# Performance work log

Hardware: AMD Instinct MI355X
Metric: run time of the kernel (lower is better)

## Reference

```python
import jax, jax.numpy as jnp
import numpy as np

B, BOUNDS, NRIM, K, UNITS = 4096, 512, 6, 4, 600
H_IN, DK_IN, DV_IN = 4, 64, 400
H_C, DK_C, DV_C = 4, 32, 100


def setup_inputs() -> dict:
    key = jax.random.key(0)
    ks = jax.random.split(key, 16)
    s = 0.02
    return {
        'inputs': jax.random.normal(ks[0], (B, BOUNDS + NRIM), jnp.float32),
        'hs': jax.random.normal(ks[1], (B, NRIM, UNITS), jnp.float32) * s,
        'cs': jax.random.normal(ks[2], (B, NRIM, UNITS), jnp.float32) * s,
        'Wk': jax.random.normal(ks[3], (BOUNDS, H_IN * DK_IN), jnp.float32) * s,
        'bk': jnp.zeros((H_IN * DK_IN,), jnp.float32),
        'Wv': jax.random.normal(ks[4], (BOUNDS, H_IN * DV_IN), jnp.float32) * s,
        'bv': jnp.zeros((H_IN * DV_IN,), jnp.float32),
        'Wq': jax.random.normal(ks[5], (NRIM, UNITS, H_IN * DK_IN), jnp.float32) * s,
        'lstm_k': jax.random.normal(ks[6], (NRIM, DV_IN, 4 * UNITS), jnp.float32) * s,
        'lstm_r': jax.random.normal(ks[7], (NRIM, UNITS, 4 * UNITS), jnp.float32) * s,
        'lstm_b': jnp.zeros((NRIM, 4 * UNITS), jnp.float32),
        'Wkc': jax.random.normal(ks[8], (NRIM, UNITS, H_C * DK_C), jnp.float32) * s,
        'Wvc': jax.random.normal(ks[9], (NRIM, UNITS, H_C * DV_C), jnp.float32) * s,
        'Wqc': jax.random.normal(ks[10], (NRIM, UNITS, H_C * DK_C), jnp.float32) * s,
        'Wout': jax.random.normal(ks[11], (NRIM, H_C * DV_C, UNITS), jnp.float32) * s,
    }


def _split_heads(t, n_heads, d_head):
    # [B, T, n_heads*d_head] -> [B, n_heads, T, d_head] (matches tf.split+stack)
    b, t_len = t.shape[0], t.shape[1]
    return t.reshape(b, t_len, n_heads, d_head).transpose(0, 2, 1, 3)


def reference(inputs, hs, cs, Wk, bk, Wv, bv, Wq, lstm_k, lstm_r, lstm_b, Wkc, Wvc, Wqc, Wout):
    x = inputs[:, :BOUNDS]                                   # [B, bounds]
    rim_dist = inputs[:, BOUNDS:BOUNDS + NRIM]               # [B, nRIM]

    # ---- input attention ----
    xx = jnp.stack([x, jnp.zeros_like(x)], axis=1)           # [B, 2, bounds]
    k_lay = xx @ Wk + bk                                     # [B, 2, H*dk]
    v_lay = xx @ Wv + bv                                     # [B, 2, H*dv]
    q_lay = jnp.einsum('bnu,nuo->bno', hs, Wq)               # grouped linear [B, nRIM, H*dq]
    kh = _split_heads(k_lay, H_IN, DK_IN)                    # [B, H, 2, dk]
    vh = _split_heads(v_lay, H_IN, DV_IN)                    # [B, H, 2, dv]
    qh = _split_heads(q_lay, H_IN, DK_IN)                    # [B, H, nRIM, dk]
    v2 = vh.mean(axis=1)                                     # [B, 2, dv]
    scores = jnp.einsum('bhnd,bhtd->bhnt', qh, kh) / np.sqrt(DK_IN).astype(np.float32)
    scores2 = scores.mean(axis=1)                            # [B, nRIM, 2]

    # top-k RIM selection mask from RIM_dist (use_attn=False path)
    _, idx = jax.lax.top_k(rim_dist, K)                      # [B, K]
    mask = jnp.zeros((inputs.shape[0], NRIM), inputs.dtype)
    mask = mask.at[jnp.arange(inputs.shape[0])[:, None], idx].set(1.0)[..., None]  # [B, nRIM, 1]

    probs = jax.nn.softmax(scores2, axis=-1)                 # dropout inactive (training=False)
    rnn_in = jnp.einsum('bnt,btv->bnv', probs, v2) * mask    # [B, nRIM, dv]

    # ---- grouped LSTM (keras gate order i,f,c,o) ----
    gates = (jnp.einsum('bnv,nvo->bno', rnn_in, lstm_k)
             + jnp.einsum('bnu,nuo->bno', hs, lstm_r) + lstm_b)  # [B, nRIM, 4*units]
    i, f, g, o = jnp.split(gates, 4, axis=-1)
    c_rnn = jax.nn.sigmoid(f) * cs + jax.nn.sigmoid(i) * jnp.tanh(g)
    h_rnn = jax.nn.sigmoid(o) * jnp.tanh(c_rnn)
    h_new = jax.lax.stop_gradient(h_rnn * (1.0 - mask)) + h_rnn * mask

    # ---- communication attention among RIMs ----
    kc = _split_heads(jnp.einsum('bnu,nuo->bno', h_new, Wkc), H_C, DK_C)  # [B, Hc, nRIM, dkc]
    vc = _split_heads(jnp.einsum('bnu,nuo->bno', h_new, Wvc), H_C, DV_C)
    qc = _split_heads(jnp.einsum('bnu,nuo->bno', h_new, Wqc), H_C, DK_C)
    sc = jnp.einsum('bhnd,bhmd->bhnm', qc, kc) / np.sqrt(DK_C).astype(np.float32)
    pc = jax.nn.softmax(sc, axis=-1) * mask[:, None, :, :]   # zero rows of inactive query RIMs
    ctx = jnp.einsum('bhnm,bhmv->bhnv', pc, vc)              # [B, Hc, nRIM, dvc]
    ctx = ctx.transpose(0, 2, 1, 3).reshape(inputs.shape[0], NRIM, H_C * DV_C)
    h_comm = jnp.einsum('bno,nou->bnu', ctx, Wout) + h_new   # grouped output proj + residual

    # ---- masked state update ----
    h_upd = h_comm * mask + hs * (1.0 - mask)
    c_upd = c_rnn * mask + cs * (1.0 - mask)
    out_state = h_upd.reshape(inputs.shape[0], UNITS * NRIM)
    return out_state, h_upd, c_upd
```

## Files before the change

### kernel.cpp

```cpp
#include <hip/hip_runtime.h>

namespace {
typedef unsigned short u16;
typedef __attribute__((ext_vector_type(8))) __bf16 bf16x8;
typedef __attribute__((ext_vector_type(4))) float f32x4;

constexpr long long kB  = 4096;
constexpr long long kOS = kB * 3600;
constexpr size_t kGAs = 4096ull * 1088;
constexpr int kHnS = 3648;

constexpr size_t oWkvT  = 0;
constexpr size_t oWqT   = oWkvT  + 768ull*512*2;
constexpr size_t oWcomT = oWqT   + 6ull*256*640*2;
constexpr size_t oWoutT = oWcomT + 6ull*768*640*2;
constexpr size_t oLstmT = oWoutT + 6ull*640*448*2;
constexpr size_t oBp    = oLstmT + 6ull*2560*1024*2;
constexpr size_t oBkv   = oBp    + 6ull*2560*4;
constexpr size_t oMask  = oBkv   + 768*4;
constexpr size_t oArena = oMask  + 4096ull*6*4;
constexpr size_t oGA    = oArena;
constexpr size_t oKV    = oGA   + 6ull*kGAs*2;
constexpr size_t oXbf   = oKV   + 4096ull*768*2;
constexpr size_t oQlay  = oXbf;
constexpr size_t oCqv   = oArena;
constexpr size_t oCtx   = oCqv  + 4096ull*4608*2;
}

__device__ __forceinline__ u16 f2b(float f) {
  union { float f; unsigned u; } x; x.f = f;
  unsigned r = (x.u + 0x7fffu + ((x.u >> 16) & 1u)) >> 16;
  return (u16)r;
}
__device__ __forceinline__ float b2f(u16 u) {
  union { unsigned u; float f; } x; x.u = ((unsigned)u) << 16;
  return x.f;
}
__device__ __forceinline__ float sigmoidf_(float x) { return 1.f / (1.f + __expf(-x)); }
__device__ __forceinline__ float tanhf_(float x) {
  const float e = __expf(2.f * x);
  return 1.f - 2.f / (e + 1.f);
}

__device__ __forceinline__ void gload16(const void* g, void* l) {
  __builtin_amdgcn_global_load_lds((const __attribute__((address_space(1))) void*)g,
                                   (__attribute__((address_space(3))) void*)l, 16, 0, 0);
}

union FragU4 { uint4 u4; bf16x8 v; };

template<int MODE>
__global__ __launch_bounds__(256, 2) void gemm64(
    const u16* __restrict__ A, int lda, long strideA,
    const u16* __restrict__ Bt, long strideB, int Kpad,
    void* __restrict__ C, int ldc, int strideC,
    const float* __restrict__ bias, int strideBias,
    int N, int nks, int storeBf16, int nx,
    const float* __restrict__ mask, float* __restrict__ h_upd,
    const float* __restrict__ hs_in, float* __restrict__ out_state)
{
  __shared__ __align__(16) u16 lds[2 * 16384];

  const int nwg = gridDim.x;
  const int orig = blockIdx.x;
  int wgid;
  {
    const int q = nwg >> 3, r = nwg & 7;
    const int xcd = orig & 7, bidx = orig >> 3;
    wgid = (xcd < r ? xcd * (q + 1) : r * (q + 1) + (xcd - r) * q) + bidx;
  }
  const int xt = wgid % nx;
  const int t2 = wgid / nx;
  const int mt = t2 & 31;
  const int rim = t2 >> 5;
  const int m0 = mt * 128, n0 = xt * 128;

  A += (size_t)rim * strideA;
  Bt += (size_t)rim * strideB;
  if (bias) bias += (size_t)rim * strideBias;

  const int t = threadIdx.x;
  const int w = t >> 6, lane = t & 63;
  const int lrow = lane & 15, lk = lane >> 4;
  const int wr = w >> 1, wc = w & 1;

  f32x4 acc[4][4] = {};

  const u16* aS[4]; const u16* bS[4]; int cC[4];
#pragma unroll
  for (int i = 0; i < 4; ++i) {
    const int c = t + i * 256;
    const int row = c >> 3, slot = c & 7;
    cC[i] = c;
    aS[i] = A  + (size_t)(m0 + row) * lda  + ((slot ^ (row & 7)) << 3);
    bS[i] = Bt + (size_t)(n0 + row) * Kpad + ((slot ^ (row & 7)) << 3);
  }
  auto stage = [&](u16* dst) {
#pragma unroll
    for (int i = 0; i < 4; ++i) gload16(aS[i], dst + (size_t)cC[i] * 8);
#pragma unroll
    for (int i = 0; i < 4; ++i) gload16(bS[i], dst + 8192 + (size_t)cC[i] * 8);
#pragma unroll
    for (int i = 0; i < 4; ++i) { aS[i] += 64; bS[i] += 64; }
  };

  stage(lds);
  asm volatile("s_waitcnt vmcnt(0)" ::: "memory");
  __builtin_amdgcn_s_barrier();

  for (int s = 0; s < nks; ++s) {
    const bool more = (s + 1 < nks);
    if (more) stage(lds + ((s + 1) & 1) * 16384);
    __builtin_amdgcn_sched_barrier(0);
    const char* Ab = (const char*)(lds + (s & 1) * 16384);
    const char* Bb = Ab + 16384;
#pragma unroll
    for (int ks = 0; ks < 2; ++ks) {
      FragU4 af[4], bf4[4];
#pragma unroll
      for (int mf = 0; mf < 4; ++mf) {
        const int rr = wr * 64 + mf * 16 + lrow;
        af[mf].u4 = *(const uint4*)(Ab + rr * 128 + ((((ks << 2) | lk) ^ (rr & 7)) << 4));
      }
#pragma unroll
      for (int nf = 0; nf < 4; ++nf) {
        const int rr = wc * 64 + nf * 16 + lrow;
        bf4[nf].u4 = *(const uint4*)(Bb + rr * 128 + ((((ks << 2) | lk) ^ (rr & 7)) << 4));
      }
#pragma unroll
      for (int mf = 0; mf < 4; ++mf)
#pragma unroll
        for (int nf = 0; nf < 4; ++nf)
          acc[mf][nf] = __builtin_amdgcn_mfma_f32_16x16x32_bf16(af[mf].v, bf4[nf].v, acc[mf][nf], 0, 0, 0);
    }
    if (more) {
      asm volatile("s_waitcnt vmcnt(0)" ::: "memory");
      __builtin_amdgcn_s_barrier();
    }
  }

  if (MODE == 0) {
    float* Cf = (float*)C + (size_t)rim * strideC;
    u16*   Cu = (u16*)C + (size_t)rim * strideC;
#pragma unroll
    for (int mf = 0; mf < 4; ++mf)
#pragma unroll
      for (int r2 = 0; r2 < 4; ++r2) {
        const int m = m0 + wr * 64 + mf * 16 + 4 * lk + r2;
#pragma unroll
        for (int nf = 0; nf < 4; ++nf) {
          const int col = n0 + wc * 64 + nf * 16 + lrow;
          if (col < N) {
            float v = acc[mf][nf][r2];
            if (bias) v += bias[col];
            const size_t off = (size_t)m * ldc + col;
            if (storeBf16) Cu[off] = f2b(v); else Cf[off] = v;
          }
        }
      }
  } else {
#pragma unroll
    for (int mf = 0; mf < 4; ++mf)
#pragma unroll
      for (int r2 = 0; r2 < 4; ++r2) {
        const int m = m0 + wr * 64 + mf * 16 + 4 * lk + r2;
        const float mk = mask[(size_t)m * 6 + rim];
#pragma unroll
        for (int nf = 0; nf < 4; ++nf) {
          const int col = n0 + wc * 64 + nf * 16 + lrow;
          if (col < 600) {
            const size_t off = (size_t)m * 3600 + rim * 600 + col;
            const float v = (mk != 0.f) ? (acc[mf][nf][r2] + h_upd[off]) : hs_in[off];
            h_upd[off] = v;
            out_state[off] = v;
          }
        }
      }
  }
}

__global__ __launch_bounds__(512, 2) void gates256(
    const u16* __restrict__ A, const u16* __restrict__ Bt,
    const float* __restrict__ bp, const float* __restrict__ cs,
    const float* __restrict__ mask,
    float* __restrict__ c_upd, float* __restrict__ h_upd, u16* __restrict__ hnbf)
{
  __shared__ __align__(16) u16 lds[2 * 32768];

  const int orig = blockIdx.x;
  const int wgid = (orig & 7) * 120 + (orig >> 3);
  const int rim = wgid / 160;
  const int rem = wgid % 160;
  const int half = rem / 80;
  const int r2d = rem % 80;
  const int mt = r2d / 5;
  const int xt = half * 5 + r2d % 5;
  const int m0 = mt * 256, n0 = xt * 256;

  const u16* Ar = A + (size_t)rim * kGAs;
  const u16* Br = Bt + (size_t)rim * (2560ull * 1024);
  const float* bip = bp + (size_t)rim * 2560;

  const int t = threadIdx.x;
  const int w = t >> 6, lane = t & 63;
  const int lrow = lane & 15, lk = lane >> 4;
  const int wr = w >> 2, wc = w & 3;

  f32x4 acc[8][4] = {};

  const u16* aP[2]; const u16* bP[2]; int dC[2];
#pragma unroll
  for (int i = 0; i < 2; ++i) {
    const int c = t + i * 512;
    const int grow = 2 * (c >> 3) + ((c >> 2) & 1);
    const int su2 = (c & 3) ^ ((c >> 3) & 3);
    dC[i] = c * 8;
    aP[i] = Ar + (size_t)(m0 + grow) * 1088 + su2 * 8;
    bP[i] = Br + (size_t)(n0 + grow) * 1024 + su2 * 8;
  }
  auto stageU = [&](int isB, int kh, int ktile, u16* buf) {
    u16* dst = buf + (isB ? 16384 : 0) + kh * 8192;
    const int go = ktile * 64 + kh * 32;
#pragma unroll
    for (int i = 0; i < 2; ++i)
      gload16((isB ? bP[i] : aP[i]) + go, dst + dC[i]);
  };

  constexpr int nks = 16;
  stageU(0, 0, 0, lds); stageU(1, 0, 0, lds); stageU(0, 1, 0, lds); stageU(1, 1, 0, lds);

  for (int T = 0; T < nks; ++T) {
    const char* tb = (const char*)(lds + (T & 1) * 32768);
    const char* Ah[2] = { tb, tb + 16384 };
    const char* Bh[2] = { tb + 32768, tb + 49152 };
    u16* nxt = lds + ((T + 1) & 1) * 32768;
    const bool st = (T + 1 < nks);

    FragU4 af[4], bfr[4];

    asm volatile("s_waitcnt vmcnt(4)\ns_barrier" ::: "memory");
    __builtin_amdgcn_sched_barrier(0);
#pragma unroll
    for (int nf = 0; nf < 4; ++nf) {
      const int rr = wc * 64 + nf * 16 + lrow;
      bfr[nf].u4 = *(const uint4*)(Bh[0] + (rr >> 1) * 128 +
                   ((((rr & 1) << 2) | (lk ^ ((rr >> 1) & 3))) << 4));
    }
#pragma unroll
    for (int mf = 0; mf < 4; ++mf) {
      const int rr = wr * 128 + mf * 16 + lrow;
      af[mf].u4 = *(const uint4*)(Ah[0] + (rr >> 1) * 128 +
                  ((((rr & 1) << 2) | (lk ^ ((rr >> 1) & 3))) << 4));
    }
    if (st) stageU(0, 0, T + 1, nxt);
    __builtin_amdgcn_s_setprio(1);
#pragma unroll
    for (int mf = 0; mf < 4; ++mf)
#pragma unroll
      for (int nf = 0; nf < 4; ++nf)
        acc[mf][nf] = __builtin_amdgcn_mfma_f32_16x16x32_bf16(af[mf].v, bfr[nf].v, acc[mf][nf], 0, 0, 0);
    __builtin_amdgcn_s_setprio(0);

#pragma unroll
    for (int mf = 0; mf < 4; ++mf) {
      const int rr = wr * 128 + 64 + mf * 16 + lrow;
      af[mf].u4 = *(const uint4*)(Ah[0] + (rr >> 1) * 128 +
                  ((((rr & 1) << 2) | (lk ^ ((rr >> 1) & 3))) << 4));
    }
    if (st) stageU(1, 0, T + 1, nxt);
    __builtin_amdgcn_s_setprio(1);
#pragma unroll
    for (int mf = 0; mf < 4; ++mf)
#pragma unroll
      for (int nf = 0; nf < 4; ++nf)
        acc[4 + mf][nf] = __builtin_amdgcn_mfma_f32_16x16x32_bf16(af[mf].v, bfr[nf].v, acc[4 + mf][nf], 0, 0, 0);
    __builtin_amdgcn_s_setprio(0);

    if (st) asm volatile("s_waitcnt vmcnt(4)\ns_barrier" ::: "memory");
    else    asm volatile("s_waitcnt vmcnt(0)\ns_barrier" ::: "memory");
    __builtin_amdgcn_sched_barrier(0);
#pragma unroll
    for (int nf = 0; nf < 4; ++nf) {
      const int rr = wc * 64 + nf * 16 + lrow;
      bfr[nf].u4 = *(const uint4*)(Bh[1] + (rr >> 1) * 128 +
                   ((((rr & 1) << 2) | (lk ^ ((rr >> 1) & 3))) << 4));
    }
#pragma unroll
    for (int mf = 0; mf < 4; ++mf) {
      const int rr = wr * 128 + mf * 16 + lrow;
      af[mf].u4 = *(const uint4*)(Ah[1] + (rr >> 1) * 128 +
                  ((((rr & 1) << 2) | (lk ^ ((rr >> 1) & 3))) << 4));
    }
    if (st) stageU(0, 1, T + 1, nxt);
    __builtin_amdgcn_s_setprio(1);
#pragma unroll
    for (int mf = 0; mf < 4; ++mf)
#pragma unroll
      for (int nf = 0; nf < 4; ++nf)
        acc[mf][nf] = __builtin_amdgcn_mfma_f32_16x16x32_bf16(af[mf].v, bfr[nf].v, acc[mf][nf], 0, 0, 0);
    __builtin_amdgcn_s_setprio(0);

#pragma unroll
    for (int mf = 0; mf < 4; ++mf) {
      const int rr = wr * 128 + 64 + mf * 16 + lrow;
      af[mf].u4 = *(const uint4*)(Ah[1] + (rr >> 1) * 128 +
                  ((((rr & 1) << 2) | (lk ^ ((rr >> 1) & 3))) << 4));
    }
    if (st) stageU(1, 1, T + 1, nxt);
    __builtin_amdgcn_s_setprio(1);
#pragma unroll
    for (int mf = 0; mf < 4; ++mf)
#pragma unroll
      for (int nf = 0; nf < 4; ++nf)
        acc[4 + mf][nf] = __builtin_amdgcn_mfma_f32_16x16x32_bf16(af[mf].v, bfr[nf].v, acc[4 + mf][nf], 0, 0, 0);
    __builtin_amdgcn_s_setprio(0);
  }

  const int nb = n0 + wc * 64;
  const int u = ((nb >> 6) << 4) + lrow;
  if (u < 600) {
    const float b_i = bip[nb + lrow];
    const float b_f = bip[nb + 16 + lrow];
    const float b_g = bip[nb + 32 + lrow];
    const float b_o = bip[nb + 48 + lrow];
#pragma unroll
    for (int mf = 0; mf < 8; ++mf)
#pragma unroll
      for (int r2 = 0; r2 < 4; ++r2) {
        const int m = m0 + wr * 128 + mf * 16 + 4 * lk + r2;
        const float iv = acc[mf][0][r2] + b_i;
        const float fv = acc[mf][1][r2] + b_f;
        const float gv = acc[mf][2][r2] + b_g;
        const float ov = acc[mf][3][r2] + b_o;
        const size_t off = (size_t)m * 3600 + rim * 600 + u;
        const float cprev = cs[off];
        const float cv = sigmoidf_(fv) * cprev + sigmoidf_(iv) * tanhf_(gv);
        const float hv = sigmoidf_(ov) * tanhf_(cv);
        const float mk = mask[(size_t)m * 6 + rim];
        c_upd[off] = (mk != 0.f) ? cv : cprev;
        h_upd[off] = hv;
        hnbf[(size_t)m * kHnS + rim * 600 + u] = f2b(hv);
      }
  }
}

__device__ void pack_wt_body(float (*tile)[65], int bx, int by, int rim,
    const float* __restrict__ i1, long s1, const float* __restrict__ i2, long s2,
    int K1, int Ktot, int ldin, int Nreal,
    u16* __restrict__ out, long so, int Kpad, int gateperm, int tid)
{
  i1 += (size_t)rim * s1;
  if (i2) i2 += (size_t)rim * s2;
  u16* o = out + (size_t)rim * so;
  const int n0 = bx * 64, k0 = by * 64;
  const int lane = tid & 63, qq = tid >> 6;
  const int n = n0 + lane;
  int col;
  if (gateperm) {
    const int g = (n >> 4) & 3, u = ((n >> 6) << 4) + (n & 15);
    col = (u < 600) ? g * 600 + u : -1;
  } else {
    col = (n < Nreal) ? n : -1;
  }
#pragma unroll
  for (int i = 0; i < 16; ++i) {
    const int kk = qq + 4 * i;
    const int k = k0 + kk;
    float v = 0.f;
    if (col >= 0) {
      if (k < K1) v = i1[(size_t)k * ldin + col];
      else if (k < Ktot) v = i2[(size_t)(k - K1) * ldin + col];
    }
    tile[kk][lane] = v;
  }
  __syncthreads();
#pragma unroll
  for (int i = 0; i < 16; ++i) {
    const int nn = qq + 4 * i;
    const int k = k0 + lane;
    if (k < Kpad) o[(size_t)(n0 + nn) * Kpad + k] = f2b(tile[lane][nn]);
  }
}

__global__ __launch_bounds__(256) void megapack_w(
    const float* __restrict__ Wk, const float* __restrict__ Wv,
    const float* __restrict__ Wkc, const float* __restrict__ Wqc, const float* __restrict__ Wvc,
    const float* __restrict__ Wq, const float* __restrict__ Wout,
    const float* __restrict__ lstm_k, const float* __restrict__ lstm_r,
    u16* __restrict__ WkvT, u16* __restrict__ WcomT, u16* __restrict__ WqT,
    u16* __restrict__ WoutT, u16* __restrict__ LstmT)
{
  __shared__ float tile[64][65];
  const int id = blockIdx.x, t = threadIdx.x;
  if (id < 3840) {
    const int bx = id % 40, by = (id / 40) % 16, bz = id / 640;
    pack_wt_body(tile, bx, by, bz, lstm_k, 400l*2400, lstm_r, 600l*2400,
                 400, 1000, 2400, 2400, LstmT, 2560l*1024, 1024, 1, t);
  } else if (id < 4260) {
    const int i2 = id - 3840;
    const int bx = i2 % 10, by = (i2 / 10) % 7, bz = i2 / 70;
    pack_wt_body(tile, bx, by, bz, Wout, 400l*600, nullptr, 0,
                 400, 400, 600, 600, WoutT, 640l*448, 448, 0, t);
  } else if (id < 4500) {
    const int i3 = id - 4260;
    const int bx = i3 % 4, by = (i3 / 4) % 10, bz = i3 / 40;
    pack_wt_body(tile, bx, by, bz, Wq, 600l*256, nullptr, 0,
                 600, 600, 256, 256, WqT, 256l*640, 640, 0, t);
  } else if (id < 4692) {
    const int e8 = ((id - 4500) * 256 + t) * 8;
    const int n = e8 >> 9, k0 = e8 & 511;
    u16 st[8];
#pragma unroll
    for (int j = 0; j < 8; ++j) {
      const int k = k0 + j;
      float v = 0.f;
      if (n < 256) v = Wk[(size_t)k * 256 + n];
      else if (n < 656) {
        const float* p = Wv + (size_t)k * 1600 + (n - 256);
        v = 0.25f * (p[0] + p[400] + p[800] + p[1200]);
      }
      st[j] = f2b(v);
    }
    *(uint4*)(WkvT + e8) = *(const uint4*)st;
  } else {
    const long long e8 = ((long long)(id - 4692) * 256 + t) * 8;
    const int rim = (int)(e8 / 491520);
    const int rem = (int)(e8 % 491520);
    const int n = rem / 640, k0 = rem % 640;
    u16 st[8];
#pragma unroll
    for (int j = 0; j < 8; ++j) {
      const int k = k0 + j;
      float v = 0.f;
      if (k < 600) {
        if (n < 128)      v = Wkc[(size_t)rim * 76800 + (size_t)k * 128 + n];
        else if (n < 256) v = Wqc[(size_t)rim * 76800 + (size_t)k * 128 + (n - 128)];
        else if (n < 656) v = Wvc[(size_t)rim * 240000 + (size_t)k * 400 + (n - 256)];
      }
      st[j] = f2b(v);
    }
    *(uint4*)(WcomT + e8) = *(const uint4*)st;
  }
}

__global__ __launch_bounds__(256) void megapack_act(
    const float* __restrict__ inputs, const float* __restrict__ hs,
    const float* __restrict__ lstm_b, const float* __restrict__ bk, const float* __restrict__ bv,
    u16* __restrict__ xbf, u16* __restrict__ gA, float* __restrict__ bp, float* __restrict__ bkv,
    u16* __restrict__ hnbf)
{
  __shared__ float row[3600];
  const int id = blockIdx.x, t = threadIdx.x;
  if (id < 4096) {
    const int b = id;
    for (int i = t; i < 3600; i += 256) row[i] = hs[(size_t)b * 3600 + i];
    __syncthreads();
    for (int c = t; c < 516; c += 256) {
      const int rim = c / 86;
      const int j = (c % 86) * 8;
      u16 v[8];
#pragma unroll
      for (int k = 0; k < 8; ++k) {
        const int col = j + k;
        v[k] = (col < 600) ? f2b(row[rim * 600 + col]) : (u16)0;
      }
      *(uint4*)(gA + (size_t)rim * kGAs + (size_t)b * 1088 + 400 + j) = *(const uint4*)v;
    }
    if (t < 6) {
      u16 z[8] = {0,0,0,0,0,0,0,0};
      *(uint4*)(hnbf + (size_t)b * kHnS + 3600 + t * 8) = *(const uint4*)z;
    }
  } else if (id < 5120) {
    const int e8 = ((id - 4096) * 256 + t) * 8;
    const int b = e8 >> 9, c0 = e8 & 511;
    const float* src = inputs + (size_t)b * 518 + c0;
    u16 st[8];
#pragma unroll
    for (int j = 0; j < 8; ++j) st[j] = f2b(src[j]);
    *(uint4*)(xbf + e8) = *(const uint4*)st;
  } else {
    const int tt = (id - 5120) * 256 + t;
    if (tt < 6 * 2560) {
      const int rim = tt / 2560, p = tt % 2560;
      const int g = (p >> 4) & 3, u = ((p >> 6) << 4) + (p & 15);
      bp[tt] = (u < 600) ? lstm_b[(size_t)rim * 2400 + g * 600 + u] : 0.f;
    }
    if (tt < 768) {
      float v = 0.f;
      if (tt < 256) v = bk[tt];
      else if (tt < 656) { const int j2 = tt - 256; v = 0.25f * (bv[j2] + bv[j2+400] + bv[j2+800] + bv[j2+1200]); }
      bkv[tt] = v;
    }
  }
}

__global__ __launch_bounds__(256) void score_kernel(
    const float* __restrict__ inputs, const u16* __restrict__ qlayb,
    const u16* __restrict__ kvb, const float* __restrict__ bk,
    const float* __restrict__ bkv,
    float* __restrict__ maskout, u16* __restrict__ gA)
{
  const int b = blockIdx.x;
  const int t = threadIdx.x;
  __shared__ float red[4][12];
  __shared__ float sprob[12];
  __shared__ float smask[6];

  const float k0v = b2f(kvb[(size_t)b * 768 + t]);
  const float bkv_ = bk[t];
  float part[12];
#pragma unroll
  for (int n = 0; n < 6; ++n) {
    const float q = b2f(qlayb[(size_t)b * 1536 + n * 256 + t]);
    part[2 * n]     = q * k0v;
    part[2 * n + 1] = q * bkv_;
  }
#pragma unroll
  for (int off = 32; off > 0; off >>= 1)
#pragma unroll
    for (int i = 0; i < 12; ++i)
      part[i] += __shfl_down(part[i], off);
  const int wave = t >> 6, lane = t & 63;
  if (lane == 0)
#pragma unroll
    for (int i = 0; i < 12; ++i) red[wave][i] = part[i];
  __syncthreads();
  if (t < 12) red[0][t] = (red[0][t] + red[1][t] + red[2][t] + red[3][t]) * (1.0f / 32.0f);
  __syncthreads();
  if (t < 6) {
    const float s0 = red[0][2 * t], s1 = red[0][2 * t + 1];
    const float mx = fmaxf(s0, s1);
    const float e0 = __expf(s0 - mx), e1 = __expf(s1 - mx);
    const float inv = 1.f / (e0 + e1);
    sprob[2 * t] = e0 * inv;
    sprob[2 * t + 1] = e1 * inv;
    const float* rd = inputs + (size_t)b * 518 + 512;
    const float mine = rd[t];
    int rank = 0;
#pragma unroll
    for (int j = 0; j < 6; ++j) {
      const float o = rd[j];
      rank += (o > mine) || (o == mine && j < t);
    }
    const float mk = (rank < 4) ? 1.f : 0.f;
    smask[t] = mk;
    maskout[(size_t)b * 6 + t] = mk;
  }
  __syncthreads();
  for (int c = t; c < 300; c += 256) {
    const int n = c / 50;
    const int v = (c % 50) * 8;
    const float p0 = sprob[2 * n], p1 = sprob[2 * n + 1], mk = smask[n];
    u16 st[8];
#pragma unroll
    for (int k = 0; k < 8; ++k)
      st[k] = f2b((p0 * b2f(kvb[(size_t)b * 768 + 256 + v + k]) + p1 * bkv[256 + v + k]) * mk);
    *reinterpret_cast<uint4*>(gA + (size_t)n * kGAs + (size_t)b * 1088 + v) =
        *reinterpret_cast<const uint4*>(st);
  }
}

__global__ __launch_bounds__(256) void comm_kernel(
    const u16* __restrict__ cqv, u16* __restrict__ ctx)
{
  const int b = blockIdx.x, t = threadIdx.x;
  __shared__ float skc[768], sqc[768], svc[2400];
  __shared__ float spc[4][6][6];
  for (int i = t * 4; i < 4608; i += 1024) {
    const ushort4 u4 = *reinterpret_cast<const ushort4*>(cqv + (size_t)b * 4608 + i);
    const u16 uu[4] = {u4.x, u4.y, u4.z, u4.w};
#pragma unroll
    for (int j = 0; j < 4; ++j) {
      const int ii = i + j;
      const int m = ii / 768, c = ii % 768;
      const float v = b2f(uu[j]);
      if (c < 128) skc[m * 128 + c] = v;
      else if (c < 256) sqc[m * 128 + (c - 128)] = v;
      else if (c < 656) svc[m * 400 + (c - 256)] = v;
    }
  }
  __syncthreads();
  if (t < 144) {
    const int h = t / 36, n = (t % 36) / 6, m = t % 6;
    float s = 0.f;
#pragma unroll
    for (int d = 0; d < 32; ++d) s += sqc[n * 128 + h * 32 + d] * skc[m * 128 + h * 32 + d];
    spc[h][n][m] = s * 0.17677669529663687f;
  }
  __syncthreads();
  if (t < 24) {
    const int h = t / 6, n = t % 6;
    float mx = -3.0e38f;
#pragma unroll
    for (int m = 0; m < 6; ++m) mx = fmaxf(mx, spc[h][n][m]);
    float e[6], sum = 0.f;
#pragma unroll
    for (int m = 0; m < 6; ++m) { e[m] = __expf(spc[h][n][m] - mx); sum += e[m]; }
    const float inv = 1.f / sum;
#pragma unroll
    for (int m = 0; m < 6; ++m) spc[h][n][m] = e[m] * inv;
  }
  __syncthreads();
  for (int base = t * 4; base < 2400; base += 1024) {
    const int n = base / 400, rr = base % 400, h = rr / 100, v = rr % 100;
    ushort4 st;
    float s0 = 0.f, s1 = 0.f, s2 = 0.f, s3 = 0.f;
#pragma unroll
    for (int m = 0; m < 6; ++m) {
      const float p = spc[h][n][m];
      const float* vm = &svc[m * 400 + h * 100 + v];
      s0 += p * vm[0]; s1 += p * vm[1]; s2 += p * vm[2]; s3 += p * vm[3];
    }
    st.x = f2b(s0); st.y = f2b(s1); st.z = f2b(s2); st.w = f2b(s3);
    *reinterpret_cast<ushort4*>(ctx + (size_t)b * 2400 + base) = st;
  }
}

extern "C" void kernel_launch(void* const* d_in, const int* in_sizes, int n_in,
                              void* d_out, int out_size, void* d_ws, size_t ws_size,
                              hipStream_t stream) {
  const float* inputs = (const float*)d_in[0];
  const float* hs     = (const float*)d_in[1];
  const float* cs     = (const float*)d_in[2];
  const float* Wk     = (const float*)d_in[3];
  const float* bk     = (const float*)d_in[4];
  const float* Wv     = (const float*)d_in[5];
  const float* bv     = (const float*)d_in[6];
  const float* Wq     = (const float*)d_in[7];
  const float* lstm_k = (const float*)d_in[8];
  const float* lstm_r = (const float*)d_in[9];
  const float* lstm_b = (const float*)d_in[10];
  const float* Wkc    = (const float*)d_in[11];
  const float* Wvc    = (const float*)d_in[12];
  const float* Wqc    = (const float*)d_in[13];
  const float* Wout   = (const float*)d_in[14];

  float* out = (float*)d_out;
  float* out_state = out;
  float* h_upd = out + kOS;
  float* c_upd = out + 2 * kOS;
  u16*   hnbf  = (u16*)d_out;

  char* wsb = (char*)d_ws;
  u16* WkvT  = (u16*)(wsb + oWkvT);
  u16* WqT   = (u16*)(wsb + oWqT);
  u16* WcomT = (u16*)(wsb + oWcomT);
  u16* WoutT = (u16*)(wsb + oWoutT);
  u16* LstmT = (u16*)(wsb + oLstmT);
  float* bp    = (float*)(wsb + oBp);
  float* bkv   = (float*)(wsb + oBkv);
  float* maskf = (float*)(wsb + oMask);
  u16* gA    = (u16*)(wsb + oGA);
  u16* kvb   = (u16*)(wsb + oKV);
  u16* xbf   = (u16*)(wsb + oXbf);
  u16* qlayb = (u16*)(wsb + oQlay);
  u16* cqvb  = (u16*)(wsb + oCqv);
  u16* ctxb  = (u16*)(wsb + oCtx);

  dim3 B256(256);

  megapack_w<<<6132, B256, 0, stream>>>(Wk, Wv, Wkc, Wqc, Wvc, Wq, Wout, lstm_k, lstm_r,
                                        WkvT, WcomT, WqT, WoutT, LstmT);
  megapack_act<<<5180, B256, 0, stream>>>(inputs, hs, lstm_b, bk, bv, xbf, gA, bp, bkv, hnbf);

  gemm64<0><<<dim3(192), B256, 0, stream>>>(xbf, 512, 0, WkvT, 0, 512,
      kvb, 768, 0, bkv, 0, 656, 8, 1, 6,
      nullptr, nullptr, nullptr, nullptr);
  gemm64<0><<<dim3(384), B256, 0, stream>>>(gA + 400, 1088, (long)kGAs, WqT, 256l*640, 640,
      qlayb, 1536, 256, nullptr, 0, 256, 10, 1, 2,
      nullptr, nullptr, nullptr, nullptr);

  score_kernel<<<4096, B256, 0, stream>>>(inputs, qlayb, kvb, bk, bkv, maskf, gA);

  gates256<<<dim3(960), dim3(512), 0, stream>>>(gA, LstmT, bp, cs, maskf, c_upd, h_upd, hnbf);

  gemm64<0><<<dim3(1152), B256, 0, stream>>>(hnbf, kHnS, 600, WcomT, 768l*640, 640,
      cqvb, 4608, 768, nullptr, 0, 656, 10, 1, 6,
      nullptr, nullptr, nullptr, nullptr);

  comm_kernel<<<4096, B256, 0, stream>>>(cqvb, ctxb);

  gemm64<1><<<dim3(960), B256, 0, stream>>>(ctxb, 2400, 400, WoutT, 640l*448, 448,
      nullptr, 0, 0, nullptr, 0, 600, 7, 0, 5,
      maskf, h_upd, hs, out_state);
}
```

Baseline: 563.0 us.

## Split A-tile staging per half and add finer-grained waits in LSTM GEMM

Reorganizes the LSTM gate GEMM's LDS staging so each A half-tile (64 rows) is loaded separately with a simpler row-linear swizzled layout, and B is staged alongside the first A half. Extra s_waitcnt/barrier points are inserted before each half's fragment reads, so the kernel waits only for the data it needs next instead of a whole k-slice. This aims to overlap global loads with MFMA work more tightly and simplify LDS address math. The cost is additional barriers per iteration and vmcnt bookkeeping that must exactly match the issue order, which is easy to get wrong.

```diff
diff --git a/kernel.cpp b/kernel.cpp
--- a/kernel.cpp
+++ b/kernel.cpp
@@ -208,51 +208,52 @@
 
   f32x4 acc[8][4] = {};
 
-  const u16* aP[2]; const u16* bP[2]; int dC[2];
+  const int aR = ((t >> 2) & 63) + (((t >> 2) >> 6) << 7);
+  const int aSu = (t & 3) ^ ((t >> 3) & 3);
+  const u16* aBase = Ar + (size_t)(m0 + aR) * 1088 + aSu * 8;
+  const u16* bBase[2];
 #pragma unroll
   for (int i = 0; i < 2; ++i) {
     const int c = t + i * 512;
-    const int grow = 2 * (c >> 3) + ((c >> 2) & 1);
-    const int su2 = (c & 3) ^ ((c >> 3) & 3);
-    dC[i] = c * 8;
-    aP[i] = Ar + (size_t)(m0 + grow) * 1088 + su2 * 8;
-    bP[i] = Br + (size_t)(n0 + grow) * 1024 + su2 * 8;
-  }
-  auto stageU = [&](int isB, int kh, int ktile, u16* buf) {
-    u16* dst = buf + (isB ? 16384 : 0) + kh * 8192;
-    const int go = ktile * 64 + kh * 32;
-#pragma unroll
-    for (int i = 0; i < 2; ++i)
-      gload16((isB ? bP[i] : aP[i]) + go, dst + dC[i]);
+    const int row = c >> 2;
+    const int su = (c & 3) ^ ((c >> 3) & 3);
+    bBase[i] = Br + (size_t)(n0 + row) * 1024 + su * 8;
+  }
+  auto stageA = [&](int h, int ks, int Tt, u16* buf) {
+    gload16(aBase + (size_t)h * 64 * 1088 + Tt * 64 + ks * 32,
+            buf + (ks * 2 + h) * 4096 + t * 8);
   };
+  auto stageB = [&](int ks, int Tt, u16* buf) {
+    gload16(bBase[0] + Tt * 64 + ks * 32, buf + 16384 + ks * 8192 + t * 8);
+    gload16(bBase[1] + Tt * 64 + ks * 32, buf + 16384 + ks * 8192 + (t + 512) * 8);
+  };
 
   constexpr int nks = 16;
-  stageU(0, 0, 0, lds); stageU(1, 0, 0, lds); stageU(0, 1, 0, lds); stageU(1, 1, 0, lds);
+  stageA(0, 0, 0, lds); stageB(0, 0, lds);
+  stageA(1, 0, 0, lds);
+  stageA(0, 1, 0, lds); stageB(1, 0, lds);
+  stageA(1, 1, 0, lds);
 
   for (int T = 0; T < nks; ++T) {
     const char* tb = (const char*)(lds + (T & 1) * 32768);
-    const char* Ah[2] = { tb, tb + 16384 };
-    const char* Bh[2] = { tb + 32768, tb + 49152 };
     u16* nxt = lds + ((T + 1) & 1) * 32768;
     const bool st = (T + 1 < nks);
 
     FragU4 af[4], bfr[4];
 
-    asm volatile("s_waitcnt vmcnt(4)\ns_barrier" ::: "memory");
+    asm volatile("s_waitcnt vmcnt(5)\ns_barrier" ::: "memory");
     __builtin_amdgcn_sched_barrier(0);
 #pragma unroll
     for (int nf = 0; nf < 4; ++nf) {
       const int rr = wc * 64 + nf * 16 + lrow;
-      bfr[nf].u4 = *(const uint4*)(Bh[0] + (rr >> 1) * 128 +
-                   ((((rr & 1) << 2) | (lk ^ ((rr >> 1) & 3))) << 4));
+      bfr[nf].u4 = *(const uint4*)(tb + 32768 + rr * 64 + ((lk ^ ((rr >> 1) & 3)) << 4));
     }
 #pragma unroll
     for (int mf = 0; mf < 4; ++mf) {
-      const int rr = wr * 128 + mf * 16 + lrow;
-      af[mf].u4 = *(const uint4*)(Ah[0] + (rr >> 1) * 128 +
-                  ((((rr & 1) << 2) | (lk ^ ((rr >> 1) & 3))) << 4));
-    }
-    if (st) stageU(0, 0, T + 1, nxt);
+      const int rp = wr * 64 + mf * 16 + lrow;
+      af[mf].u4 = *(const uint4*)(tb + rp * 64 + ((lk ^ ((rp >> 1) & 3)) << 4));
+    }
+    if (st) { stageA(0, 0, T + 1, nxt); stageB(0, T + 1, nxt); }
     __builtin_amdgcn_s_setprio(1);
 #pragma unroll
     for (int mf = 0; mf < 4; ++mf)
@@ -261,13 +262,15 @@
         acc[mf][nf] = __builtin_amdgcn_mfma_f32_16x16x32_bf16(af[mf].v, bfr[nf].v, acc[mf][nf], 0, 0, 0);
     __builtin_amdgcn_s_setprio(0);
 
+    if (st) asm volatile("s_waitcnt vmcnt(7)\ns_barrier" ::: "memory");
+    else    asm volatile("s_waitcnt vmcnt(4)\ns_barrier" ::: "memory");
+    __builtin_amdgcn_sched_barrier(0);
 #pragma unroll
     for (int mf = 0; mf < 4; ++mf) {
-      const int rr = wr * 128 + 64 + mf * 16 + lrow;
-      af[mf].u4 = *(const uint4*)(Ah[0] + (rr >> 1) * 128 +
-                  ((((rr & 1) << 2) | (lk ^ ((rr >> 1) & 3))) << 4));
-    }
-    if (st) stageU(1, 0, T + 1, nxt);
+      const int rp = wr * 64 + mf * 16 + lrow;
+      af[mf].u4 = *(const uint4*)(tb + 8192 + rp * 64 + ((lk ^ ((rp >> 1) & 3)) << 4));
+    }
+    if (st) stageA(1, 0, T + 1, nxt);
     __builtin_amdgcn_s_setprio(1);
 #pragma unroll
     for (int mf = 0; mf < 4; ++mf)
@@ -276,22 +279,20 @@
         acc[4 + mf][nf] = __builtin_amdgcn_mfma_f32_16x16x32_bf16(af[mf].v, bfr[nf].v, acc[4 + mf][nf], 0, 0, 0);
     __builtin_amdgcn_s_setprio(0);
 
-    if (st) asm volatile("s_waitcnt vmcnt(4)\ns_barrier" ::: "memory");
-    else    asm volatile("s_waitcnt vmcnt(0)\ns_barrier" ::: "memory");
+    if (st) asm volatile("s_waitcnt vmcnt(5)\ns_barrier" ::: "memory");
+    else    asm volatile("s_waitcnt vmcnt(1)\ns_barrier" ::: "memory");
     __builtin_amdgcn_sched_barrier(0);
 #pragma unroll
     for (int nf = 0; nf < 4; ++nf) {
       const int rr = wc * 64 + nf * 16 + lrow;
-      bfr[nf].u4 = *(const uint4*)(Bh[1] + (rr >> 1) * 128 +
-                   ((((rr & 1) << 2) | (lk ^ ((rr >> 1) & 3))) << 4));
+      bfr[nf].u4 = *(const uint4*)(tb + 49152 + rr * 64 + ((lk ^ ((rr >> 1) & 3)) << 4));
     }
 #pragma unroll
     for (int mf = 0; mf < 4; ++mf) {
-      const int rr = wr * 128 + mf * 16 + lrow;
-      af[mf].u4 = *(const uint4*)(Ah[1] + (rr >> 1) * 128 +
-                  ((((rr & 1) << 2) | (lk ^ ((rr >> 1) & 3))) << 4));
-    }
-    if (st) stageU(0, 1, T + 1, nxt);
+      const int rp = wr * 64 + mf * 16 + lrow;
+      af[mf].u4 = *(const uint4*)(tb + 16384 + rp * 64 + ((lk ^ ((rp >> 1) & 3)) << 4));
+    }
+    if (st) { stageA(0, 1, T + 1, nxt); stageB(1, T + 1, nxt); }
     __builtin_amdgcn_s_setprio(1);
 #pragma unroll
     for (int mf = 0; mf < 4; ++mf)
@@ -300,13 +301,15 @@
         acc[mf][nf] = __builtin_amdgcn_mfma_f32_16x16x32_bf16(af[mf].v, bfr[nf].v, acc[mf][nf], 0, 0, 0);
     __builtin_amdgcn_s_setprio(0);
 
+    if (st) asm volatile("s_waitcnt vmcnt(7)\ns_barrier" ::: "memory");
+    else    asm volatile("s_waitcnt vmcnt(0)\ns_barrier" ::: "memory");
+    __builtin_amdgcn_sched_barrier(0);
 #pragma unroll
     for (int mf = 0; mf < 4; ++mf) {
-      const int rr = wr * 128 + 64 + mf * 16 + lrow;
-      af[mf].u4 = *(const uint4*)(Ah[1] + (rr >> 1) * 128 +
-                  ((((rr & 1) << 2) | (lk ^ ((rr >> 1) & 3))) << 4));
-    }
-    if (st) stageU(1, 1, T + 1, nxt);
+      const int rp = wr * 64 + mf * 16 + lrow;
+      af[mf].u4 = *(const uint4*)(tb + 24576 + rp * 64 + ((lk ^ ((rp >> 1) & 3)) << 4));
+    }
+    if (st) stageA(1, 1, T + 1, nxt);
     __builtin_amdgcn_s_setprio(1);
 #pragma unroll
     for (int mf = 0; mf < 4; ++mf)
@@ -324,14 +327,14 @@
     const float b_g = bip[nb + 32 + lrow];
     const float b_o = bip[nb + 48 + lrow];
 #pragma unroll
-    for (int mf = 0; mf < 8; ++mf)
+    for (int idx = 0; idx < 8; ++idx)
 #pragma unroll
       for (int r2 = 0; r2 < 4; ++r2) {
-        const int m = m0 + wr * 128 + mf * 16 + 4 * lk + r2;
-        const float iv = acc[mf][0][r2] + b_i;
-        const float fv = acc[mf][1][r2] + b_f;
-        const float gv = acc[mf][2][r2] + b_g;
-        const float ov = acc[mf][3][r2] + b_o;
+        const int m = m0 + wr * 128 + (idx >> 2) * 64 + (idx & 3) * 16 + 4 * lk + r2;
+        const float iv = acc[idx][0][r2] + b_i;
+        const float fv = acc[idx][1][r2] + b_f;
+        const float gv = acc[idx][2][r2] + b_g;
+        const float ov = acc[idx][3][r2] + b_o;
         const size_t off = (size_t)m * 3600 + rim * 600 + u;
         const float cprev = cs[off];
         const float cv = sigmoidf_(fv) * cprev + sigmoidf_(iv) * tanhf_(gv);
```

After: 572.6 us. Within noise of the previous version (+1.7%).
